# Kernel tuning notes

Measured on AMD Instinct MI355X. Metric: run time of the kernel, lower is better.

## Reference

```python
import jax, jax.numpy as jnp
import numpy as np

SEQ_LEN, BATCH, D_IN, D_H, D_OUT = 512, 64, 1024, 1024, 1024
W_SCALE = 0.02  # small init so sigmoid/tanh stay in a sane range


def setup_inputs() -> dict:
    key = jax.random.key(0)
    ks = jax.random.split(key, 12)
    rn = lambda k, shape: jax.random.normal(k, shape, dtype=jnp.float32)
    return {
        "x_seq": rn(ks[0], (SEQ_LEN, BATCH, D_IN)),
        "h0": jnp.zeros((BATCH, D_H), dtype=jnp.float32),
        "Wxz_w": rn(ks[1], (D_H, D_IN)) * W_SCALE,
        "Wxz_b": rn(ks[2], (D_H,)) * W_SCALE,
        "Whz_w": rn(ks[3], (D_H, D_H)) * W_SCALE,
        "Wxr_w": rn(ks[4], (D_H, D_IN)) * W_SCALE,
        "Wxr_b": rn(ks[5], (D_H,)) * W_SCALE,
        "Whr_w": rn(ks[6], (D_H, D_H)) * W_SCALE,
        "Wxn_w": rn(ks[7], (D_H, D_IN)) * W_SCALE,
        "Wxn_b": rn(ks[8], (D_H,)) * W_SCALE,
        "Whn_w": rn(ks[9], (D_H, D_H)) * W_SCALE,
        "Why_w": rn(ks[10], (D_OUT, D_H)) * W_SCALE,
        "Why_b": rn(ks[11], (D_OUT,)) * W_SCALE,
    }


def reference(x_seq, h0, Wxz_w, Wxz_b, Whz_w, Wxr_w, Wxr_b, Whr_w,
              Wxn_w, Wxn_b, Whn_w, Why_w, Why_b):
    # Precompute all input projections in one batched GEMM per gate:
    # (S, B, D_in) @ (D_in, D_h) -> (S, B, D_h). torch Linear: x @ W.T + b.
    xz = jnp.einsum('sbi,hi->sbh', x_seq, Wxz_w) + Wxz_b
    xr = jnp.einsum('sbi,hi->sbh', x_seq, Wxr_w) + Wxr_b
    xn = jnp.einsum('sbi,hi->sbh', x_seq, Wxn_w) + Wxn_b

    def step(h, xs):
        xz_t, xr_t, xn_t = xs
        z = jax.nn.sigmoid(xz_t + h @ Whz_w.T)
        r = jax.nn.sigmoid(xr_t + h @ Whr_w.T)
        n = jnp.tanh(xn_t + (r * h) @ Whn_w.T)
        h_new = (1.0 - z) * h + z * n
        return h_new, h_new

    h_last, hs = jax.lax.scan(step, h0, (xz, xr, xn))  # hs: (S, B, D_h)
    outputs = jnp.einsum('sbh,oh->sbo', hs, Why_w) + Why_b
    return outputs, h_last
```

## Files before the change

### kernel.cpp

```cpp
#include <hip/hip_runtime.h>

typedef unsigned int uint;
typedef unsigned short ushort;

typedef short s8v __attribute__((ext_vector_type(8)));
typedef float f4v __attribute__((ext_vector_type(4)));

#define S_LEN 512
#define BATCH 64
#define DH    1024
#define DIN   1024

union B8 { s8v v; uint u[4]; unsigned long long ull[2]; ushort s[8]; };

__device__ inline ushort f2bf(float f){
  uint u = __builtin_bit_cast(uint, f);
  u += 0x7fffu + ((u >> 16) & 1u);
  return (ushort)(u >> 16);
}
__device__ inline float bf2f(ushort s){
  uint u = ((uint)s) << 16;
  return __builtin_bit_cast(float, u);
}

__device__ inline f4v mfma16(s8v a, s8v b, f4v c){
  return __builtin_amdgcn_mfma_f32_16x16x32_bf16(a, b, c, 0, 0, 0);
}

__device__ inline s8v ld_b8(const ushort* p){
  return *reinterpret_cast<const s8v*>(p);
}

__device__ inline s8v ld_b8_llc(const ushort* p){
  B8 b;
  const unsigned long long* q = (const unsigned long long*)p;
  b.ull[0] = __hip_atomic_load(q,   __ATOMIC_RELAXED, __HIP_MEMORY_SCOPE_AGENT);
  b.ull[1] = __hip_atomic_load(q+1, __ATOMIC_RELAXED, __HIP_MEMORY_SCOPE_AGENT);
  return b.v;
}

__device__ inline s8v cvt8(float4 a, float4 b){
  B8 r;
  r.s[0]=f2bf(a.x); r.s[1]=f2bf(a.y); r.s[2]=f2bf(a.z); r.s[3]=f2bf(a.w);
  r.s[4]=f2bf(b.x); r.s[5]=f2bf(b.y); r.s[6]=f2bf(b.z); r.s[7]=f2bf(b.w);
  return r.v;
}

__global__ void cvt_kernel(const float* __restrict__ src, ushort* __restrict__ dst, int n){
  int i = (blockIdx.x * blockDim.x + threadIdx.x) * 4;
  if (i + 3 < n){
    float4 v = *reinterpret_cast<const float4*>(src + i);
    unsigned long long p = (unsigned long long)f2bf(v.x)
                         | ((unsigned long long)f2bf(v.y) << 16)
                         | ((unsigned long long)f2bf(v.z) << 32)
                         | ((unsigned long long)f2bf(v.w) << 48);
    *reinterpret_cast<unsigned long long*>(dst + i) = p;
  }
}

__global__ void __launch_bounds__(256, 1)
proj3_kernel(const float* __restrict__ X,
             const ushort* __restrict__ W0, const ushort* __restrict__ W1, const ushort* __restrict__ W2,
             const float* __restrict__ bias0, const float* __restrict__ bias1, const float* __restrict__ bias2,
             ushort* __restrict__ C0, ushort* __restrict__ C1, ushort* __restrict__ C2)
{
  const int lane = threadIdx.x & 63;
  const int wave = threadIdx.x >> 6;
  const int l15  = lane & 15;
  const int krow = (lane >> 4) << 3;
  const int n0 = blockIdx.x * 64;
  const int m0 = blockIdx.y * 128 + wave * 32;

  const ushort* Ws[3] = {W0, W1, W2};
  const float*  Bs[3] = {bias0, bias1, bias2};
  ushort*       Cs[3] = {C0, C1, C2};

  f4v acc[2][3][4];
  #pragma unroll
  for (int ms = 0; ms < 2; ++ms)
    #pragma unroll
    for (int g = 0; g < 3; ++g)
      #pragma unroll
      for (int nn = 0; nn < 4; ++nn)
        acc[ms][g][nn] = (f4v){0.f,0.f,0.f,0.f};

  const float* a0 = X + (m0 + l15) * DIN + krow;
  const float* a1 = a0 + 16 * DIN;

  for (int k = 0; k < DIN; k += 32){
    s8v af[2];
    {
      const float4* p0 = reinterpret_cast<const float4*>(a0 + k);
      const float4* p1 = reinterpret_cast<const float4*>(a1 + k);
      af[0] = cvt8(p0[0], p0[1]);
      af[1] = cvt8(p1[0], p1[1]);
    }
    #pragma unroll
    for (int g = 0; g < 3; ++g){
      const ushort* W = Ws[g];
      #pragma unroll
      for (int nn = 0; nn < 4; ++nn){
        s8v bfr = ld_b8(W + (n0 + nn*16 + l15) * DIN + k + krow);
        acc[0][g][nn] = mfma16(af[0], bfr, acc[0][g][nn]);
        acc[1][g][nn] = mfma16(af[1], bfr, acc[1][g][nn]);
      }
    }
  }

  #pragma unroll
  for (int g = 0; g < 3; ++g){
    ushort* C = Cs[g];
    #pragma unroll
    for (int nn = 0; nn < 4; ++nn){
      const int n = n0 + nn*16 + l15;
      const float bv = Bs[g][n];
      #pragma unroll
      for (int ms = 0; ms < 2; ++ms){
        #pragma unroll
        for (int r = 0; r < 4; ++r){
          int m = m0 + ms*16 + ((lane>>4)<<2) + r;
          C[m * DH + n] = f2bf(acc[ms][g][nn][r] + bv);
        }
      }
    }
  }
}

__global__ void __launch_bounds__(256, 1)
gemm1_kernel(const ushort* __restrict__ A, const ushort* __restrict__ W,
             const float* __restrict__ bias, float* __restrict__ C)
{
  const int lane = threadIdx.x & 63;
  const int wave = threadIdx.x >> 6;
  const int l15  = lane & 15;
  const int krow = (lane >> 4) << 3;
  const int n0 = blockIdx.x * 128;
  const int m0 = blockIdx.y * 128 + wave * 32;

  f4v acc[2][8];
  #pragma unroll
  for (int ms = 0; ms < 2; ++ms)
    #pragma unroll
    for (int nn = 0; nn < 8; ++nn)
      acc[ms][nn] = (f4v){0.f,0.f,0.f,0.f};

  const ushort* a0 = A + (m0 + l15) * DH + krow;
  const ushort* a1 = a0 + 16 * DH;

  for (int k = 0; k < DH; k += 32){
    s8v af0 = ld_b8(a0 + k);
    s8v af1 = ld_b8(a1 + k);
    #pragma unroll
    for (int nn = 0; nn < 8; ++nn){
      s8v b = ld_b8(W + (n0 + nn*16 + l15) * DH + k + krow);
      acc[0][nn] = mfma16(af0, b, acc[0][nn]);
      acc[1][nn] = mfma16(af1, b, acc[1][nn]);
    }
  }

  #pragma unroll
  for (int nn = 0; nn < 8; ++nn){
    const int n = n0 + nn*16 + l15;
    const float bv = bias[n];
    #pragma unroll
    for (int ms = 0; ms < 2; ++ms){
      #pragma unroll
      for (int r = 0; r < 4; ++r){
        int m = m0 + ms*16 + ((lane>>4)<<2) + r;
        C[m * DH + n] = acc[ms][nn][r] + bv;
      }
    }
  }
}

__global__ void __launch_bounds__(256, 1)
scan_kernel(const ushort* __restrict__ xz, const ushort* __restrict__ xr,
            const ushort* __restrict__ xn,
            const ushort* __restrict__ Whz, const ushort* __restrict__ Whr,
            const ushort* __restrict__ Whn,
            const float* __restrict__ h0,
            ushort* __restrict__ hbuf,
            ushort* __restrict__ rhbuf,
            ushort* __restrict__ hs,
            float*  __restrict__ hlast,
            uint* __restrict__ hflags,
            uint* __restrict__ rhflags)
{
  const int tid  = threadIdx.x;
  const int wid  = blockIdx.x;
  const int g    = wid >> 6;
  const int jt   = wid & 63;
  const int b0   = g * 16;
  const int j0   = jt * 16;
  const int wave = tid >> 6;
  const int lane = tid & 63;
  const int l15  = lane & 15;
  const int krow = (lane >> 4) << 3;
  const int kbase = wave * 256;

  s8v wz[8], wr[8], wn[8];
  {
    const int wrow = j0 + l15;
    #pragma unroll
    for (int kk = 0; kk < 8; ++kk){
      int off = wrow * DH + kbase + kk*32 + krow;
      wz[kk] = ld_b8(Whz + off);
      wr[kk] = ld_b8(Whr + off);
      wn[kk] = ld_b8(Whn + off);
    }
  }

  const int bl = tid >> 4;
  const int jl = tid & 15;
  const int brow = b0 + bl;
  const int jcol = j0 + jl;
  const int arow = b0 + l15;

  __shared__ float red[8][256];

  float h = h0[brow * DH + jcol];
  {
    ushort mybf = f2bf(h);
    uint other = (uint)(ushort)__shfl_xor((int)mybf, 1, 64);
    if ((tid & 1) == 0){
      uint pack = (uint)mybf | (other << 16);
      uint* dst = (uint*)(hbuf + 64*1024 + brow*DH + jcol);
      __hip_atomic_store(dst, pack, __ATOMIC_RELAXED, __HIP_MEMORY_SCOPE_AGENT);
    }
  }
  __syncthreads();
  if (tid == 0)
    __hip_atomic_store(&hflags[wid*4], 1u, __ATOMIC_RELAXED, __HIP_MEMORY_SCOPE_AGENT);

  float zreg = 0.f;

  #pragma unroll 1
  for (int t = 0; t < S_LEN; ++t){
    {
      const uint* fp = hflags + (g*64 + wave*16 + l15) * 4;
      const uint tgt = (uint)(t + 1);
      while (true){
        uint v = __hip_atomic_load(fp, __ATOMIC_RELAXED, __HIP_MEMORY_SCOPE_AGENT);
        if (__all(v >= tgt)) break;
        __builtin_amdgcn_s_sleep(2);
      }
    }
    __asm__ volatile("" ::: "memory");

    const int xidx = (t * BATCH + brow) * DH + jcol;
    float xzv = bf2f(xz[xidx]);
    float xrv = bf2f(xr[xidx]);

    f4v accz = (f4v){0.f,0.f,0.f,0.f};
    f4v accr = (f4v){0.f,0.f,0.f,0.f};
    {
      const ushort* ap = hbuf + ((t ^ 1) & 1) * (64*1024) + arow * DH + kbase + krow;
      #pragma unroll
      for (int kk = 0; kk < 8; ++kk){
        s8v a = ld_b8_llc(ap + kk*32);
        accz = mfma16(a, wz[kk], accz);
        accr = mfma16(a, wr[kk], accr);
      }
    }
    {
      int base = ((lane >> 4) * 4) * 16 + l15;
      #pragma unroll
      for (int r = 0; r < 4; ++r){
        red[wave][base + r*16]   = accz[r];
        red[4+wave][base + r*16] = accr[r];
      }
    }
    __syncthreads();
    float sz = red[0][tid] + red[1][tid] + red[2][tid] + red[3][tid];
    float sr = red[4][tid] + red[5][tid] + red[6][tid] + red[7][tid];
    float z = 1.f / (1.f + __expf(-(xzv + sz)));
    float r = 1.f / (1.f + __expf(-(xrv + sr)));
    zreg = z;
    float rh = r * h;
    {
      ushort mybf = f2bf(rh);
      uint other = (uint)(ushort)__shfl_xor((int)mybf, 1, 64);
      if ((tid & 1) == 0){
        uint pack = (uint)mybf | (other << 16);
        uint* dst = (uint*)(rhbuf + (t & 1)*(64*1024) + brow*DH + jcol);
        __hip_atomic_store(dst, pack, __ATOMIC_RELAXED, __HIP_MEMORY_SCOPE_AGENT);
      }
    }
    __syncthreads();
    if (tid == 0)
      __hip_atomic_store(&rhflags[wid*4], (uint)(t+1), __ATOMIC_RELAXED, __HIP_MEMORY_SCOPE_AGENT);

    {
      const uint* fp = rhflags + (g*64 + wave*16 + l15) * 4;
      const uint tgt = (uint)(t + 1);
      while (true){
        uint v = __hip_atomic_load(fp, __ATOMIC_RELAXED, __HIP_MEMORY_SCOPE_AGENT);
        if (__all(v >= tgt)) break;
        __builtin_amdgcn_s_sleep(2);
      }
    }
    __asm__ volatile("" ::: "memory");

    float xnv = bf2f(xn[xidx]);
    f4v accn = (f4v){0.f,0.f,0.f,0.f};
    {
      const ushort* ap = rhbuf + (t & 1)*(64*1024) + arow * DH + kbase + krow;
      #pragma unroll
      for (int kk = 0; kk < 8; ++kk){
        s8v a = ld_b8_llc(ap + kk*32);
        accn = mfma16(a, wn[kk], accn);
      }
    }
    {
      int base = ((lane >> 4) * 4) * 16 + l15;
      #pragma unroll
      for (int r4 = 0; r4 < 4; ++r4)
        red[wave][base + r4*16] = accn[r4];
    }
    __syncthreads();
    float sn = red[0][tid] + red[1][tid] + red[2][tid] + red[3][tid];
    float pre = xnv + sn;
    float e = __expf(2.f * pre);
    float n = 1.f - 2.f / (e + 1.f);
    float hnew = h + zreg * (n - h);
    h = hnew;
    {
      ushort mybf = f2bf(hnew);
      uint other = (uint)(ushort)__shfl_xor((int)mybf, 1, 64);
      if ((tid & 1) == 0){
        uint pack = (uint)mybf | (other << 16);
        uint* dst = (uint*)(hbuf + (t & 1)*(64*1024) + brow*DH + jcol);
        __hip_atomic_store(dst, pack, __ATOMIC_RELAXED, __HIP_MEMORY_SCOPE_AGENT);
      }
      hs[xidx] = mybf;
      if (t == S_LEN-1) hlast[brow*DH + jcol] = hnew;
    }
    __syncthreads();
    if (tid == 0)
      __hip_atomic_store(&hflags[wid*4], (uint)(t+2), __ATOMIC_RELAXED, __HIP_MEMORY_SCOPE_AGENT);
  }
}

extern "C" void kernel_launch(void* const* d_in, const int* in_sizes, int n_in,
                              void* d_out, int out_size, void* d_ws, size_t ws_size,
                              hipStream_t stream) {
  const float* x_seq = (const float*)d_in[0];
  const float* h0    = (const float*)d_in[1];
  const float* Wxz_w = (const float*)d_in[2];
  const float* Wxz_b = (const float*)d_in[3];
  const float* Whz_w = (const float*)d_in[4];
  const float* Wxr_w = (const float*)d_in[5];
  const float* Wxr_b = (const float*)d_in[6];
  const float* Whr_w = (const float*)d_in[7];
  const float* Wxn_w = (const float*)d_in[8];
  const float* Wxn_b = (const float*)d_in[9];
  const float* Whn_w = (const float*)d_in[10];
  const float* Why_w = (const float*)d_in[11];
  const float* Why_b = (const float*)d_in[12];

  const size_t MiB = 1u << 20;
  unsigned char* ws = (unsigned char*)d_ws;

  ushort* Whz16 = (ushort*)(ws + 0*MiB);
  ushort* Whr16 = (ushort*)(ws + 2*MiB);
  ushort* Whn16 = (ushort*)(ws + 4*MiB);
  ushort* Wxz16 = (ushort*)(ws + 6*MiB);
  ushort* Wxr16 = (ushort*)(ws + 8*MiB);
  ushort* Wxn16 = (ushort*)(ws + 10*MiB);
  ushort* Why16 = (ushort*)(ws + 12*MiB);
  ushort* xn_buf = (ushort*)(ws + 16*MiB);
  ushort* hs     = (ushort*)(ws + 80*MiB);
  ushort* hbuf   = (ushort*)(ws + 144*MiB);
  ushort* rhbuf  = (ushort*)(ws + 144*MiB + 256*1024);
  uint*   hflags = (uint*)  (ws + 144*MiB + 512*1024);
  uint*   rhflags= (uint*)  (ws + 144*MiB + 516*1024);

  ushort* xz_buf = (ushort*)d_out;
  ushort* xr_buf = xz_buf + (size_t)S_LEN*BATCH*DH;
  float*  out_f  = (float*)d_out;
  float*  hlast  = out_f + (size_t)S_LEN*BATCH*DH;

  const int NW = DH * DIN;

  cvt_kernel<<<1024, 256, 0, stream>>>(Whz_w, Whz16, NW);
  cvt_kernel<<<1024, 256, 0, stream>>>(Whr_w, Whr16, NW);
  cvt_kernel<<<1024, 256, 0, stream>>>(Whn_w, Whn16, NW);
  cvt_kernel<<<1024, 256, 0, stream>>>(Wxz_w, Wxz16, NW);
  cvt_kernel<<<1024, 256, 0, stream>>>(Wxr_w, Wxr16, NW);
  cvt_kernel<<<1024, 256, 0, stream>>>(Wxn_w, Wxn16, NW);
  cvt_kernel<<<1024, 256, 0, stream>>>(Why_w, Why16, NW);

  proj3_kernel<<<dim3(16, 256), 256, 0, stream>>>(
      x_seq, Wxz16, Wxr16, Wxn16, Wxz_b, Wxr_b, Wxn_b, xz_buf, xr_buf, xn_buf);

  hipMemsetAsync((void*)hflags, 0, 8192, stream);

  scan_kernel<<<256, 256, 0, stream>>>(
      xz_buf, xr_buf, xn_buf, Whz16, Whr16, Whn16, h0,
      hbuf, rhbuf, hs, hlast, hflags, rhflags);

  gemm1_kernel<<<dim3(8, 256), 256, 0, stream>>>(hs, Why16, Why_b, out_f);
}
```

Before: 6.527 ms.

## Replace per-block flag barriers with per-element tagged values in scan

The recurrent scan kernel stops publishing h and r*h through separate data buffers plus per-block flags. Each element is now a 32-bit word holding a timestep tag and the bf16 value, and consumers poll the data words directly until every tag is current. This removes the syncthreads-then-flag-store handshake and the separate flag polling, so dependencies resolve per fragment instead of per block. The cost is twice the bytes read and written per h exchange, extra unpacking work, and a bounded spin guard that could silently continue with stale data if it ever triggers.

```diff
diff --git a/kernel.cpp b/kernel.cpp
--- a/kernel.cpp
+++ b/kernel.cpp
@@ -2,6 +2,7 @@
 
 typedef unsigned int uint;
 typedef unsigned short ushort;
+typedef unsigned long long u64;
 
 typedef short s8v __attribute__((ext_vector_type(8)));
 typedef float f4v __attribute__((ext_vector_type(4)));
@@ -11,7 +12,7 @@
 #define DH    1024
 #define DIN   1024
 
-union B8 { s8v v; uint u[4]; unsigned long long ull[2]; ushort s[8]; };
+union B8 { s8v v; uint u[4]; u64 ull[2]; ushort s[8]; };
 
 __device__ inline ushort f2bf(float f){
   uint u = __builtin_bit_cast(uint, f);
@@ -31,12 +32,11 @@
   return *reinterpret_cast<const s8v*>(p);
 }
 
-__device__ inline s8v ld_b8_llc(const ushort* p){
-  B8 b;
-  const unsigned long long* q = (const unsigned long long*)p;
-  b.ull[0] = __hip_atomic_load(q,   __ATOMIC_RELAXED, __HIP_MEMORY_SCOPE_AGENT);
-  b.ull[1] = __hip_atomic_load(q+1, __ATOMIC_RELAXED, __HIP_MEMORY_SCOPE_AGENT);
-  return b.v;
+__device__ inline u64 ald(const uint* p){
+  return __hip_atomic_load((const u64*)p, __ATOMIC_RELAXED, __HIP_MEMORY_SCOPE_AGENT);
+}
+__device__ inline void ast(uint* p, uint v){
+  __hip_atomic_store(p, v, __ATOMIC_RELAXED, __HIP_MEMORY_SCOPE_AGENT);
 }
 
 __device__ inline s8v cvt8(float4 a, float4 b){
@@ -46,16 +46,78 @@
   return r.v;
 }
 
+__device__ inline s8v extract8(const u64 w[4]){
+  B8 o;
+  #pragma unroll
+  for (int i = 0; i < 4; ++i)
+    o.u[i] = (uint)(w[i] & 0xFFFFull) | (((uint)(w[i] >> 32)) << 16);
+  return o.v;
+}
+
+__device__ inline bool tags_ok2(u64 w, uint tag){
+  return ((((uint)(w >> 16)) & 0xFFFFu) >= tag) & (((uint)(w >> 48)) >= tag);
+}
+
+template<int NF>
+__device__ inline void poll_frags(const uint* __restrict__ base, uint tag, u64 (&aw)[NF][4]){
+  u64 pr[NF];
+  #pragma unroll
+  for (int i = 0; i < NF; ++i) pr[i] = ald(base + i*32);
+  int guard = 0;
+  while (true){
+    uint np = 0;
+    #pragma unroll
+    for (int i = 0; i < NF; ++i) if (!tags_ok2(pr[i], tag)) np |= (1u << i);
+    if (__all(np == 0)) break;
+    if (++guard > (1 << 16)) break;
+    __builtin_amdgcn_s_sleep(4);
+    #pragma unroll
+    for (int i = 0; i < NF; ++i) if ((np >> i) & 1u) pr[i] = ald(base + i*32);
+  }
+  #pragma unroll
+  for (int i = 0; i < NF; ++i){
+    aw[i][0] = pr[i];
+    #pragma unroll
+    for (int j = 1; j < 4; ++j) aw[i][j] = ald(base + i*32 + j*2);
+  }
+  uint pend = (uint)((1u << NF) - 1u);
+  guard = 0;
+  while (true){
+    uint np = 0;
+    #pragma unroll
+    for (int i = 0; i < NF; ++i)
+      if ((pend >> i) & 1u){
+        bool ok = tags_ok2(aw[i][0], tag) & tags_ok2(aw[i][1], tag)
+                & tags_ok2(aw[i][2], tag) & tags_ok2(aw[i][3], tag);
+        if (!ok) np |= (1u << i);
+      }
+    pend = np;
+    if (__all(pend == 0)) break;
+    if (++guard > (1 << 16)) break;
+    #pragma unroll
+    for (int i = 0; i < NF; ++i)
+      if ((pend >> i) & 1u){
+        #pragma unroll
+        for (int j = 0; j < 4; ++j) aw[i][j] = ald(base + i*32 + j*2);
+      }
+  }
+}
+
 __global__ void cvt_kernel(const float* __restrict__ src, ushort* __restrict__ dst, int n){
   int i = (blockIdx.x * blockDim.x + threadIdx.x) * 4;
   if (i + 3 < n){
     float4 v = *reinterpret_cast<const float4*>(src + i);
-    unsigned long long p = (unsigned long long)f2bf(v.x)
-                         | ((unsigned long long)f2bf(v.y) << 16)
-                         | ((unsigned long long)f2bf(v.z) << 32)
-                         | ((unsigned long long)f2bf(v.w) << 48);
-    *reinterpret_cast<unsigned long long*>(dst + i) = p;
-  }
+    u64 p = (u64)f2bf(v.x)
+          | ((u64)f2bf(v.y) << 16)
+          | ((u64)f2bf(v.z) << 32)
+          | ((u64)f2bf(v.w) << 48);
+    *reinterpret_cast<u64*>(dst + i) = p;
+  }
+}
+
+__global__ void h0pack_kernel(const float* __restrict__ h0, uint* __restrict__ htag){
+  int i = blockIdx.x * blockDim.x + threadIdx.x;
+  htag[i] = (1u << 16) | (uint)f2bf(h0[i]);
 }
 
 __global__ void __launch_bounds__(256, 1)
@@ -179,34 +241,31 @@
             const ushort* __restrict__ Whz, const ushort* __restrict__ Whr,
             const ushort* __restrict__ Whn,
             const float* __restrict__ h0,
-            ushort* __restrict__ hbuf,
-            ushort* __restrict__ rhbuf,
-            ushort* __restrict__ hs,
-            float*  __restrict__ hlast,
-            uint* __restrict__ hflags,
-            uint* __restrict__ rhflags)
+            uint* __restrict__ htag, uint* __restrict__ rhtag,
+            ushort* __restrict__ hs, float* __restrict__ hlast)
 {
   const int tid  = threadIdx.x;
-  const int wid  = blockIdx.x;
-  const int g    = wid >> 6;
-  const int jt   = wid & 63;
-  const int b0   = g * 16;
-  const int j0   = jt * 16;
   const int wave = tid >> 6;
   const int lane = tid & 63;
   const int l15  = lane & 15;
-  const int krow = (lane >> 4) << 3;
-  const int kbase = wave * 256;
+  const int hi2  = lane >> 4;
+  const int krow = hi2 << 3;
+  const int wid  = blockIdx.x;
+  const int b0   = (wid >> 6) << 4;
+  const int j0   = (wid & 63) << 4;
+  const int kbase = wave << 8;
+
+  __shared__ float redA[8][256];
+  __shared__ float redB[4][256];
 
   s8v wz[8], wr[8], wn[8];
   {
-    const int wrow = j0 + l15;
+    const int wbase = (j0 + l15) * DH + kbase + krow;
     #pragma unroll
     for (int kk = 0; kk < 8; ++kk){
-      int off = wrow * DH + kbase + kk*32 + krow;
-      wz[kk] = ld_b8(Whz + off);
-      wr[kk] = ld_b8(Whr + off);
-      wn[kk] = ld_b8(Whn + off);
+      wz[kk] = ld_b8(Whz + wbase + kk*32);
+      wr[kk] = ld_b8(Whr + wbase + kk*32);
+      wn[kk] = ld_b8(Whn + wbase + kk*32);
     }
   }
 
@@ -214,130 +273,83 @@
   const int jl = tid & 15;
   const int brow = b0 + bl;
   const int jcol = j0 + jl;
-  const int arow = b0 + l15;
-
-  __shared__ float red[8][256];
-
   float h = h0[brow * DH + jcol];
-  {
-    ushort mybf = f2bf(h);
-    uint other = (uint)(ushort)__shfl_xor((int)mybf, 1, 64);
-    if ((tid & 1) == 0){
-      uint pack = (uint)mybf | (other << 16);
-      uint* dst = (uint*)(hbuf + 64*1024 + brow*DH + jcol);
-      __hip_atomic_store(dst, pack, __ATOMIC_RELAXED, __HIP_MEMORY_SCOPE_AGENT);
-    }
-  }
-  __syncthreads();
-  if (tid == 0)
-    __hip_atomic_store(&hflags[wid*4], 1u, __ATOMIC_RELAXED, __HIP_MEMORY_SCOPE_AGENT);
-
+
+  const uint* hpoll  = htag  + (b0 + l15)*DH + kbase + krow;
+  const uint* rhpoll = rhtag + (b0 + l15)*DH + kbase + krow;
+  uint* rhdst = rhtag + brow*DH + jcol;
+  uint* hdst  = htag  + brow*DH + jcol;
+
+  const int lbase = hi2*64 + l15;
+
+  u64 aw[8][4];
   float zreg = 0.f;
 
   #pragma unroll 1
   for (int t = 0; t < S_LEN; ++t){
-    {
-      const uint* fp = hflags + (g*64 + wave*16 + l15) * 4;
-      const uint tgt = (uint)(t + 1);
-      while (true){
-        uint v = __hip_atomic_load(fp, __ATOMIC_RELAXED, __HIP_MEMORY_SCOPE_AGENT);
-        if (__all(v >= tgt)) break;
-        __builtin_amdgcn_s_sleep(2);
-      }
-    }
-    __asm__ volatile("" ::: "memory");
-
-    const int xidx = (t * BATCH + brow) * DH + jcol;
+    const int xidx = (t*BATCH + brow)*DH + jcol;
+
     float xzv = bf2f(xz[xidx]);
     float xrv = bf2f(xr[xidx]);
 
-    f4v accz = (f4v){0.f,0.f,0.f,0.f};
-    f4v accr = (f4v){0.f,0.f,0.f,0.f};
-    {
-      const ushort* ap = hbuf + ((t ^ 1) & 1) * (64*1024) + arow * DH + kbase + krow;
-      #pragma unroll
-      for (int kk = 0; kk < 8; ++kk){
-        s8v a = ld_b8_llc(ap + kk*32);
-        accz = mfma16(a, wz[kk], accz);
-        accr = mfma16(a, wr[kk], accr);
-      }
-    }
-    {
-      int base = ((lane >> 4) * 4) * 16 + l15;
-      #pragma unroll
-      for (int r = 0; r < 4; ++r){
-        red[wave][base + r*16]   = accz[r];
-        red[4+wave][base + r*16] = accr[r];
-      }
+    poll_frags<8>(hpoll, (uint)(t + 1), aw);
+
+    f4v az0={0.f,0.f,0.f,0.f}, az1={0.f,0.f,0.f,0.f};
+    f4v ar0={0.f,0.f,0.f,0.f}, ar1={0.f,0.f,0.f,0.f};
+    #pragma unroll
+    for (int i = 0; i < 8; i += 2){
+      s8v a0 = extract8(aw[i]);
+      s8v a1 = extract8(aw[i+1]);
+      az0 = mfma16(a0, wz[i],   az0);
+      ar0 = mfma16(a0, wr[i],   ar0);
+      az1 = mfma16(a1, wz[i+1], az1);
+      ar1 = mfma16(a1, wr[i+1], ar1);
+    }
+
+    #pragma unroll
+    for (int r = 0; r < 4; ++r){
+      redA[wave][lbase + r*16]   = az0[r] + az1[r];
+      redA[4+wave][lbase + r*16] = ar0[r] + ar1[r];
     }
     __syncthreads();
-    float sz = red[0][tid] + red[1][tid] + red[2][tid] + red[3][tid];
-    float sr = red[4][tid] + red[5][tid] + red[6][tid] + red[7][tid];
+
+    float sz = redA[0][tid] + redA[1][tid] + redA[2][tid] + redA[3][tid];
+    float sr = redA[4][tid] + redA[5][tid] + redA[6][tid] + redA[7][tid];
     float z = 1.f / (1.f + __expf(-(xzv + sz)));
     float r = 1.f / (1.f + __expf(-(xrv + sr)));
     zreg = z;
     float rh = r * h;
-    {
-      ushort mybf = f2bf(rh);
-      uint other = (uint)(ushort)__shfl_xor((int)mybf, 1, 64);
-      if ((tid & 1) == 0){
-        uint pack = (uint)mybf | (other << 16);
-        uint* dst = (uint*)(rhbuf + (t & 1)*(64*1024) + brow*DH + jcol);
-        __hip_atomic_store(dst, pack, __ATOMIC_RELAXED, __HIP_MEMORY_SCOPE_AGENT);
-      }
-    }
+    ast(rhdst, (((uint)(t + 1)) << 16) | (uint)f2bf(rh));
+
+    float xnv = bf2f(xn[xidx]);
+
+    poll_frags<8>(rhpoll, (uint)(t + 1), aw);
+
+    f4v an0={0.f,0.f,0.f,0.f}, an1={0.f,0.f,0.f,0.f};
+    #pragma unroll
+    for (int i = 0; i < 8; i += 2){
+      s8v a0 = extract8(aw[i]);
+      s8v a1 = extract8(aw[i+1]);
+      an0 = mfma16(a0, wn[i],   an0);
+      an1 = mfma16(a1, wn[i+1], an1);
+    }
+
+    #pragma unroll
+    for (int r4 = 0; r4 < 4; ++r4)
+      redB[wave][lbase + r4*16] = an0[r4] + an1[r4];
     __syncthreads();
-    if (tid == 0)
-      __hip_atomic_store(&rhflags[wid*4], (uint)(t+1), __ATOMIC_RELAXED, __HIP_MEMORY_SCOPE_AGENT);
-
-    {
-      const uint* fp = rhflags + (g*64 + wave*16 + l15) * 4;
-      const uint tgt = (uint)(t + 1);
-      while (true){
-        uint v = __hip_atomic_load(fp, __ATOMIC_RELAXED, __HIP_MEMORY_SCOPE_AGENT);
-        if (__all(v >= tgt)) break;
-        __builtin_amdgcn_s_sleep(2);
-      }
-    }
-    __asm__ volatile("" ::: "memory");
-
-    float xnv = bf2f(xn[xidx]);
-    f4v accn = (f4v){0.f,0.f,0.f,0.f};
-    {
-      const ushort* ap = rhbuf + (t & 1)*(64*1024) + arow * DH + kbase + krow;
-      #pragma unroll
-      for (int kk = 0; kk < 8; ++kk){
-        s8v a = ld_b8_llc(ap + kk*32);
-        accn = mfma16(a, wn[kk], accn);
-      }
-    }
-    {
-      int base = ((lane >> 4) * 4) * 16 + l15;
-      #pragma unroll
-      for (int r4 = 0; r4 < 4; ++r4)
-        red[wave][base + r4*16] = accn[r4];
-    }
-    __syncthreads();
-    float sn = red[0][tid] + red[1][tid] + red[2][tid] + red[3][tid];
+
+    float sn = redB[0][tid] + redB[1][tid] + redB[2][tid] + redB[3][tid];
     float pre = xnv + sn;
     float e = __expf(2.f * pre);
-    float n = 1.f - 2.f / (e + 1.f);
-    float hnew = h + zreg * (n - h);
+    float nv = 1.f - 2.f / (e + 1.f);
+    float hnew = h + zreg * (nv - h);
     h = hnew;
-    {
-      ushort mybf = f2bf(hnew);
-      uint other = (uint)(ushort)__shfl_xor((int)mybf, 1, 64);
-      if ((tid & 1) == 0){
-        uint pack = (uint)mybf | (other << 16);
-        uint* dst = (uint*)(hbuf + (t & 1)*(64*1024) + brow*DH + jcol);
-        __hip_atomic_store(dst, pack, __ATOMIC_RELAXED, __HIP_MEMORY_SCOPE_AGENT);
-      }
-      hs[xidx] = mybf;
-      if (t == S_LEN-1) hlast[brow*DH + jcol] = hnew;
-    }
-    __syncthreads();
-    if (tid == 0)
-      __hip_atomic_store(&hflags[wid*4], (uint)(t+2), __ATOMIC_RELAXED, __HIP_MEMORY_SCOPE_AGENT);
+
+    ushort hbf = f2bf(hnew);
+    ast(hdst, (((uint)(t + 2)) << 16) | (uint)hbf);
+    hs[xidx] = hbf;
+    if (t == S_LEN - 1) hlast[brow*DH + jcol] = hnew;
   }
 }
 
@@ -370,10 +382,8 @@
   ushort* Why16 = (ushort*)(ws + 12*MiB);
   ushort* xn_buf = (ushort*)(ws + 16*MiB);
   ushort* hs     = (ushort*)(ws + 80*MiB);
-  ushort* hbuf   = (ushort*)(ws + 144*MiB);
-  ushort* rhbuf  = (ushort*)(ws + 144*MiB + 256*1024);
-  uint*   hflags = (uint*)  (ws + 144*MiB + 512*1024);
-  uint*   rhflags= (uint*)  (ws + 144*MiB + 516*1024);
+  uint*   htag   = (uint*)  (ws + 144*MiB);
+  uint*   rhtag  = (uint*)  (ws + 144*MiB + 256*1024);
 
   ushort* xz_buf = (ushort*)d_out;
   ushort* xr_buf = xz_buf + (size_t)S_LEN*BATCH*DH;
@@ -393,11 +403,12 @@
   proj3_kernel<<<dim3(16, 256), 256, 0, stream>>>(
       x_seq, Wxz16, Wxr16, Wxn16, Wxz_b, Wxr_b, Wxn_b, xz_buf, xr_buf, xn_buf);
 
-  hipMemsetAsync((void*)hflags, 0, 8192, stream);
+  hipMemsetAsync((void*)rhtag, 0, (size_t)BATCH*DH*sizeof(uint), stream);
+  h0pack_kernel<<<256, 256, 0, stream>>>(h0, htag);
 
   scan_kernel<<<256, 256, 0, stream>>>(
       xz_buf, xr_buf, xn_buf, Whz16, Whr16, Whn16, h0,
-      hbuf, rhbuf, hs, hlast, hflags, rhflags);
+      htag, rhtag, hs, hlast);
 
   gemm1_kernel<<<dim3(8, 256), 256, 0, stream>>>(hs, Why16, Why_b, out_f);
 }
```

After: 7.923 ms. +21.4%, slower.

## Halve scan workgroups by giving each block 32 hidden columns

Applied to the files above, without the earlier changes.

The persistent GRU scan kernel now runs 128 workgroups instead of 256, with each one covering 32 hidden columns (two 16-wide MFMA tiles) and keeping twice as many recurrent weight registers. Each thread handles two adjacent columns, so the bf16 pack no longer needs a shuffle. The x-projection loads are hoisted ahead of the flag spin-waits, and the flag arrays are resized to match. The aim is to halve the number of cross-block flags each wave polls and to cut per-step synchronisation overhead, at the cost of more MFMA work per block and higher register pressure.

```diff
diff --git a/kernel.cpp b/kernel.cpp
--- a/kernel.cpp
+++ b/kernel.cpp
@@ -2,6 +2,7 @@
 
 typedef unsigned int uint;
 typedef unsigned short ushort;
+typedef unsigned long long u64;
 
 typedef short s8v __attribute__((ext_vector_type(8)));
 typedef float f4v __attribute__((ext_vector_type(4)));
@@ -11,7 +12,7 @@
 #define DH    1024
 #define DIN   1024
 
-union B8 { s8v v; uint u[4]; unsigned long long ull[2]; ushort s[8]; };
+union B8 { s8v v; uint u[4]; u64 ull[2]; ushort s[8]; };
 
 __device__ inline ushort f2bf(float f){
   uint u = __builtin_bit_cast(uint, f);
@@ -33,10 +34,17 @@
 
 __device__ inline s8v ld_b8_llc(const ushort* p){
   B8 b;
-  const unsigned long long* q = (const unsigned long long*)p;
+  const u64* q = (const u64*)p;
   b.ull[0] = __hip_atomic_load(q,   __ATOMIC_RELAXED, __HIP_MEMORY_SCOPE_AGENT);
   b.ull[1] = __hip_atomic_load(q+1, __ATOMIC_RELAXED, __HIP_MEMORY_SCOPE_AGENT);
   return b.v;
+}
+
+__device__ inline uint ald32(const uint* p){
+  return __hip_atomic_load(p, __ATOMIC_RELAXED, __HIP_MEMORY_SCOPE_AGENT);
+}
+__device__ inline void ast32(uint* p, uint v){
+  __hip_atomic_store(p, v, __ATOMIC_RELAXED, __HIP_MEMORY_SCOPE_AGENT);
 }
 
 __device__ inline s8v cvt8(float4 a, float4 b){
@@ -50,11 +58,11 @@
   int i = (blockIdx.x * blockDim.x + threadIdx.x) * 4;
   if (i + 3 < n){
     float4 v = *reinterpret_cast<const float4*>(src + i);
-    unsigned long long p = (unsigned long long)f2bf(v.x)
-                         | ((unsigned long long)f2bf(v.y) << 16)
-                         | ((unsigned long long)f2bf(v.z) << 32)
-                         | ((unsigned long long)f2bf(v.w) << 48);
-    *reinterpret_cast<unsigned long long*>(dst + i) = p;
+    u64 p = (u64)f2bf(v.x)
+          | ((u64)f2bf(v.y) << 16)
+          | ((u64)f2bf(v.z) << 32)
+          | ((u64)f2bf(v.w) << 48);
+    *reinterpret_cast<u64*>(dst + i) = p;
   }
 }
 
@@ -187,157 +195,173 @@
             uint* __restrict__ rhflags)
 {
   const int tid  = threadIdx.x;
-  const int wid  = blockIdx.x;
-  const int g    = wid >> 6;
-  const int jt   = wid & 63;
-  const int b0   = g * 16;
-  const int j0   = jt * 16;
   const int wave = tid >> 6;
   const int lane = tid & 63;
   const int l15  = lane & 15;
-  const int krow = (lane >> 4) << 3;
-  const int kbase = wave * 256;
-
-  s8v wz[8], wr[8], wn[8];
+  const int hi2  = lane >> 4;
+  const int krow = hi2 << 3;
+  const int wid  = blockIdx.x;
+  const int g    = wid >> 5;
+  const int jt   = wid & 31;
+  const int b0   = g << 4;
+  const int j0   = jt << 5;
+  const int kbase = wave << 8;
+
+  __shared__ float redA[2][4][512];
+  __shared__ float redB[4][512];
+
+  s8v wz[2][8], wr[2][8], wn[2][8];
+  #pragma unroll
+  for (int nn = 0; nn < 2; ++nn){
+    const int wbase = (j0 + nn*16 + l15) * DH + kbase + krow;
+    #pragma unroll
+    for (int kk = 0; kk < 8; ++kk){
+      wz[nn][kk] = ld_b8(Whz + wbase + kk*32);
+      wr[nn][kk] = ld_b8(Whr + wbase + kk*32);
+      wn[nn][kk] = ld_b8(Whn + wbase + kk*32);
+    }
+  }
+
+  const int bl   = tid >> 4;
+  const int jl2  = (tid & 15) << 1;
+  const int brow = b0 + bl;
+  const int jcol = j0 + jl2;
+  float2 h2 = *reinterpret_cast<const float2*>(h0 + brow * DH + jcol);
+  float hr0 = h2.x, hr1 = h2.y;
+
+  const int arow = b0 + l15;
+  const uint* hfp  = hflags  + (g*32 + wave*8 + (l15 & 7)) * 4;
+  const uint* rhfp = rhflags + (g*32 + wave*8 + (l15 & 7)) * 4;
+  uint* rhdst = (uint*)(rhbuf) ;
+  (void)rhdst;
+
   {
-    const int wrow = j0 + l15;
-    #pragma unroll
-    for (int kk = 0; kk < 8; ++kk){
-      int off = wrow * DH + kbase + kk*32 + krow;
-      wz[kk] = ld_b8(Whz + off);
-      wr[kk] = ld_b8(Whr + off);
-      wn[kk] = ld_b8(Whn + off);
-    }
-  }
-
-  const int bl = tid >> 4;
-  const int jl = tid & 15;
-  const int brow = b0 + bl;
-  const int jcol = j0 + jl;
-  const int arow = b0 + l15;
-
-  __shared__ float red[8][256];
-
-  float h = h0[brow * DH + jcol];
-  {
-    ushort mybf = f2bf(h);
-    uint other = (uint)(ushort)__shfl_xor((int)mybf, 1, 64);
-    if ((tid & 1) == 0){
-      uint pack = (uint)mybf | (other << 16);
-      uint* dst = (uint*)(hbuf + 64*1024 + brow*DH + jcol);
-      __hip_atomic_store(dst, pack, __ATOMIC_RELAXED, __HIP_MEMORY_SCOPE_AGENT);
-    }
+    uint pack = (uint)f2bf(hr0) | ((uint)f2bf(hr1) << 16);
+    ast32((uint*)(hbuf + 64*1024 + brow*DH + jcol), pack);
   }
   __syncthreads();
   if (tid == 0)
-    __hip_atomic_store(&hflags[wid*4], 1u, __ATOMIC_RELAXED, __HIP_MEMORY_SCOPE_AGENT);
-
-  float zreg = 0.f;
+    ast32(&hflags[wid*4], 1u);
+
+  float z0 = 0.f, z1 = 0.f;
 
   #pragma unroll 1
   for (int t = 0; t < S_LEN; ++t){
-    {
-      const uint* fp = hflags + (g*64 + wave*16 + l15) * 4;
+    const int xidx = (t * BATCH + brow) * DH + jcol;
+
+    uint xzp = *reinterpret_cast<const uint*>(xz + xidx);
+    uint xrp = *reinterpret_cast<const uint*>(xr + xidx);
+    float xzv0 = bf2f((ushort)(xzp & 0xFFFFu)), xzv1 = bf2f((ushort)(xzp >> 16));
+    float xrv0 = bf2f((ushort)(xrp & 0xFFFFu)), xrv1 = bf2f((ushort)(xrp >> 16));
+
+    {
       const uint tgt = (uint)(t + 1);
       while (true){
-        uint v = __hip_atomic_load(fp, __ATOMIC_RELAXED, __HIP_MEMORY_SCOPE_AGENT);
+        uint v = ald32(hfp);
         if (__all(v >= tgt)) break;
         __builtin_amdgcn_s_sleep(2);
       }
     }
     __asm__ volatile("" ::: "memory");
 
-    const int xidx = (t * BATCH + brow) * DH + jcol;
-    float xzv = bf2f(xz[xidx]);
-    float xrv = bf2f(xr[xidx]);
-
-    f4v accz = (f4v){0.f,0.f,0.f,0.f};
-    f4v accr = (f4v){0.f,0.f,0.f,0.f};
+    f4v az[2] = {(f4v){0.f,0.f,0.f,0.f}, (f4v){0.f,0.f,0.f,0.f}};
+    f4v ar[2] = {(f4v){0.f,0.f,0.f,0.f}, (f4v){0.f,0.f,0.f,0.f}};
     {
       const ushort* ap = hbuf + ((t ^ 1) & 1) * (64*1024) + arow * DH + kbase + krow;
       #pragma unroll
       for (int kk = 0; kk < 8; ++kk){
         s8v a = ld_b8_llc(ap + kk*32);
-        accz = mfma16(a, wz[kk], accz);
-        accr = mfma16(a, wr[kk], accr);
-      }
-    }
-    {
-      int base = ((lane >> 4) * 4) * 16 + l15;
+        az[0] = mfma16(a, wz[0][kk], az[0]);
+        az[1] = mfma16(a, wz[1][kk], az[1]);
+        ar[0] = mfma16(a, wr[0][kk], ar[0]);
+        ar[1] = mfma16(a, wr[1][kk], ar[1]);
+      }
+    }
+    #pragma unroll
+    for (int nn = 0; nn < 2; ++nn)
       #pragma unroll
       for (int r = 0; r < 4; ++r){
-        red[wave][base + r*16]   = accz[r];
-        red[4+wave][base + r*16] = accr[r];
-      }
-    }
+        const int e = (hi2*4 + r)*32 + nn*16 + l15;
+        redA[0][wave][e] = az[nn][r];
+        redA[1][wave][e] = ar[nn][r];
+      }
     __syncthreads();
-    float sz = red[0][tid] + red[1][tid] + red[2][tid] + red[3][tid];
-    float sr = red[4][tid] + red[5][tid] + red[6][tid] + red[7][tid];
-    float z = 1.f / (1.f + __expf(-(xzv + sz)));
-    float r = 1.f / (1.f + __expf(-(xrv + sr)));
-    zreg = z;
-    float rh = r * h;
-    {
-      ushort mybf = f2bf(rh);
-      uint other = (uint)(ushort)__shfl_xor((int)mybf, 1, 64);
-      if ((tid & 1) == 0){
-        uint pack = (uint)mybf | (other << 16);
-        uint* dst = (uint*)(rhbuf + (t & 1)*(64*1024) + brow*DH + jcol);
-        __hip_atomic_store(dst, pack, __ATOMIC_RELAXED, __HIP_MEMORY_SCOPE_AGENT);
-      }
+
+    const int e0 = bl*32 + jl2;
+    float sz0 = redA[0][0][e0]   + redA[0][1][e0]   + redA[0][2][e0]   + redA[0][3][e0];
+    float sz1 = redA[0][0][e0+1] + redA[0][1][e0+1] + redA[0][2][e0+1] + redA[0][3][e0+1];
+    float sr0 = redA[1][0][e0]   + redA[1][1][e0]   + redA[1][2][e0]   + redA[1][3][e0];
+    float sr1 = redA[1][0][e0+1] + redA[1][1][e0+1] + redA[1][2][e0+1] + redA[1][3][e0+1];
+    z0 = 1.f / (1.f + __expf(-(xzv0 + sz0)));
+    z1 = 1.f / (1.f + __expf(-(xzv1 + sz1)));
+    float r0 = 1.f / (1.f + __expf(-(xrv0 + sr0)));
+    float r1 = 1.f / (1.f + __expf(-(xrv1 + sr1)));
+    float rh0 = r0 * hr0;
+    float rh1 = r1 * hr1;
+    {
+      uint pack = (uint)f2bf(rh0) | ((uint)f2bf(rh1) << 16);
+      ast32((uint*)(rhbuf + (t & 1)*(64*1024) + brow*DH + jcol), pack);
     }
     __syncthreads();
     if (tid == 0)
-      __hip_atomic_store(&rhflags[wid*4], (uint)(t+1), __ATOMIC_RELAXED, __HIP_MEMORY_SCOPE_AGENT);
-
-    {
-      const uint* fp = rhflags + (g*64 + wave*16 + l15) * 4;
+      ast32(&rhflags[wid*4], (uint)(t + 1));
+
+    uint xnp = *reinterpret_cast<const uint*>(xn + xidx);
+    float xnv0 = bf2f((ushort)(xnp & 0xFFFFu)), xnv1 = bf2f((ushort)(xnp >> 16));
+
+    {
       const uint tgt = (uint)(t + 1);
       while (true){
-        uint v = __hip_atomic_load(fp, __ATOMIC_RELAXED, __HIP_MEMORY_SCOPE_AGENT);
+        uint v = ald32(rhfp);
         if (__all(v >= tgt)) break;
         __builtin_amdgcn_s_sleep(2);
       }
     }
     __asm__ volatile("" ::: "memory");
 
-    float xnv = bf2f(xn[xidx]);
-    f4v accn = (f4v){0.f,0.f,0.f,0.f};
+    f4v an[2] = {(f4v){0.f,0.f,0.f,0.f}, (f4v){0.f,0.f,0.f,0.f}};
     {
       const ushort* ap = rhbuf + (t & 1)*(64*1024) + arow * DH + kbase + krow;
       #pragma unroll
       for (int kk = 0; kk < 8; ++kk){
         s8v a = ld_b8_llc(ap + kk*32);
-        accn = mfma16(a, wn[kk], accn);
-      }
-    }
-    {
-      int base = ((lane >> 4) * 4) * 16 + l15;
-      #pragma unroll
-      for (int r4 = 0; r4 < 4; ++r4)
-        red[wave][base + r4*16] = accn[r4];
-    }
+        an[0] = mfma16(a, wn[0][kk], an[0]);
+        an[1] = mfma16(a, wn[1][kk], an[1]);
+      }
+    }
+    #pragma unroll
+    for (int nn = 0; nn < 2; ++nn)
+      #pragma unroll
+      for (int r = 0; r < 4; ++r){
+        const int e = (hi2*4 + r)*32 + nn*16 + l15;
+        redB[wave][e] = an[nn][r];
+      }
     __syncthreads();
-    float sn = red[0][tid] + red[1][tid] + red[2][tid] + red[3][tid];
-    float pre = xnv + sn;
-    float e = __expf(2.f * pre);
-    float n = 1.f - 2.f / (e + 1.f);
-    float hnew = h + zreg * (n - h);
-    h = hnew;
-    {
-      ushort mybf = f2bf(hnew);
-      uint other = (uint)(ushort)__shfl_xor((int)mybf, 1, 64);
-      if ((tid & 1) == 0){
-        uint pack = (uint)mybf | (other << 16);
-        uint* dst = (uint*)(hbuf + (t & 1)*(64*1024) + brow*DH + jcol);
-        __hip_atomic_store(dst, pack, __ATOMIC_RELAXED, __HIP_MEMORY_SCOPE_AGENT);
-      }
-      hs[xidx] = mybf;
-      if (t == S_LEN-1) hlast[brow*DH + jcol] = hnew;
+
+    float sn0 = redB[0][e0]   + redB[1][e0]   + redB[2][e0]   + redB[3][e0];
+    float sn1 = redB[0][e0+1] + redB[1][e0+1] + redB[2][e0+1] + redB[3][e0+1];
+    float pre0 = xnv0 + sn0;
+    float pre1 = xnv1 + sn1;
+    float e_0 = __expf(2.f * pre0);
+    float e_1 = __expf(2.f * pre1);
+    float n0 = 1.f - 2.f / (e_0 + 1.f);
+    float n1 = 1.f - 2.f / (e_1 + 1.f);
+    float hn0 = hr0 + z0 * (n0 - hr0);
+    float hn1 = hr1 + z1 * (n1 - hr1);
+    hr0 = hn0; hr1 = hn1;
+
+    {
+      uint pack = (uint)f2bf(hn0) | ((uint)f2bf(hn1) << 16);
+      ast32((uint*)(hbuf + (t & 1)*(64*1024) + brow*DH + jcol), pack);
+      *reinterpret_cast<uint*>(hs + xidx) = pack;
+      if (t == S_LEN - 1){
+        float2 hl; hl.x = hn0; hl.y = hn1;
+        *reinterpret_cast<float2*>(hlast + brow*DH + jcol) = hl;
+      }
     }
     __syncthreads();
     if (tid == 0)
-      __hip_atomic_store(&hflags[wid*4], (uint)(t+2), __ATOMIC_RELAXED, __HIP_MEMORY_SCOPE_AGENT);
+      ast32(&hflags[wid*4], (uint)(t + 2));
   }
 }
 
@@ -373,7 +397,7 @@
   ushort* hbuf   = (ushort*)(ws + 144*MiB);
   ushort* rhbuf  = (ushort*)(ws + 144*MiB + 256*1024);
   uint*   hflags = (uint*)  (ws + 144*MiB + 512*1024);
-  uint*   rhflags= (uint*)  (ws + 144*MiB + 516*1024);
+  uint*   rhflags= (uint*)  (ws + 144*MiB + 512*1024 + 2048);
 
   ushort* xz_buf = (ushort*)d_out;
   ushort* xr_buf = xz_buf + (size_t)S_LEN*BATCH*DH;
@@ -393,9 +417,9 @@
   proj3_kernel<<<dim3(16, 256), 256, 0, stream>>>(
       x_seq, Wxz16, Wxr16, Wxn16, Wxz_b, Wxr_b, Wxn_b, xz_buf, xr_buf, xn_buf);
 
-  hipMemsetAsync((void*)hflags, 0, 8192, stream);
-
-  scan_kernel<<<256, 256, 0, stream>>>(
+  hipMemsetAsync((void*)hflags, 0, 4096, stream);
+
+  scan_kernel<<<128, 256, 0, stream>>>(
       xz_buf, xr_buf, xn_buf, Whz16, Whr16, Whn16, h0,
       hbuf, rhbuf, hs, hlast, hflags, rhflags);
 
```

New measurement: 5.563 ms. 1.17x faster.
